# Performance work log

Measured on AMD Instinct MI355X. Metric: run time of the kernel, lower is better.

The kernel has to match this reference:

```python
import jax, jax.numpy as jnp
import numpy as np
from jax import lax

B, C, HW = 128, 32, 16
N_E = 4096
PNS = (1, 2, 3, 4, 5, 6, 8, 10, 13, 16)
SN = len(PNS)
BETA, RESI = 0.25, 0.5
EPS = 1e-12

# PhiPartiallyShared tick schedule (K=4): which of the 4 Phi convs each scale uses
_TICKS = np.linspace(1.0 / 12.0, 1.0 - 1.0 / 12.0, 4)
PHI_IDX = [int(np.argmin(np.abs(_TICKS - si / (SN - 1)))) for si in range(SN)]


def _cubic_w(t, a=-0.75):
    # PyTorch bicubic kernel (a = -0.75)
    t = np.abs(t)
    return np.where(t <= 1.0, ((a + 2.0) * t - (a + 3.0)) * t * t + 1.0,
                    np.where(t < 2.0, (((t - 5.0) * t + 8.0) * t - 4.0) * a, 0.0))


def _bicubic_mat(n_in, n_out):
    # 1D resize matrix matching F.interpolate(mode='bicubic', align_corners=False)
    M = np.zeros((n_out, n_in), np.float32)
    scale = n_in / n_out
    for i in range(n_out):
        src = (i + 0.5) * scale - 0.5
        i0 = int(np.floor(src))
        f = src - i0
        for off in (-1, 0, 1, 2):
            w = float(_cubic_w(f - off))
            j = min(max(i0 + off, 0), n_in - 1)  # border replicate
            M[i, j] += w
    return M


def _area_mat(n_in, n_out):
    # 1D matrix matching F.interpolate(mode='area') == adaptive_avg_pool
    M = np.zeros((n_out, n_in), np.float32)
    for i in range(n_out):
        s = (i * n_in) // n_out
        e = -(-((i + 1) * n_in) // n_out)  # ceil
        M[i, s:e] = 1.0 / (e - s)
    return M


DOWN = {pn: jnp.asarray(_area_mat(HW, pn)) for pn in PNS[:-1]}
UP = {pn: jnp.asarray(_bicubic_mat(pn, HW)) for pn in PNS[:-1]}


def _resize2(x, M):
    # separable 2D resize: x [B,C,Y,X] -> [B,C,O,P]
    return jnp.einsum('oy,px,bcyx->bcop', M, M, x)


def _phi(h, w, b):
    conv = lax.conv_general_dilated(h, w, (1, 1), ((1, 1), (1, 1)),
                                    dimension_numbers=('NCHW', 'OIHW', 'NCHW'))
    conv = conv + b[None, :, None, None]
    return h * (1.0 - RESI) + conv * RESI


def _forward(f_input, codebook, phi_w, phi_b):
    f_ng = lax.stop_gradient(f_input)
    f_rest = f_ng
    f_hat = jnp.zeros_like(f_ng)
    cb_n = codebook / jnp.maximum(jnp.linalg.norm(codebook, axis=-1, keepdims=True), EPS)
    loss = jnp.asarray(0.0, jnp.float32)
    idx = None
    for si, pn in enumerate(PNS):
        x = _resize2(f_rest, DOWN[pn]) if si != SN - 1 else f_rest
        rest = x.transpose(0, 2, 3, 1).reshape(-1, C)          # [B*pn*pn, C]
        rest_n = rest / jnp.maximum(jnp.linalg.norm(rest, axis=-1, keepdims=True), EPS)
        idx = jnp.argmax(rest_n @ cb_n.T, axis=1)              # cosine-sim argmax
        h = codebook[idx].reshape(B, pn, pn, C).transpose(0, 3, 1, 2)
        if si != SN - 1:
            h = _resize2(h, UP[pn])
        k = PHI_IDX[si]
        h = _phi(h, phi_w[k], phi_b[k])
        f_hat = f_hat + h
        f_rest = f_rest - h
        loss = loss + BETA * jnp.mean((lax.stop_gradient(f_hat) - f_input) ** 2) \
                    + jnp.mean((f_hat - f_ng) ** 2)
    loss = loss / SN
    # straight-through estimator
    f_hat_st = f_input + lax.stop_gradient(f_hat - f_input)
    return f_hat_st, loss, idx


def setup_inputs() -> dict:
    key = jax.random.key(0)
    k1, k2, k3, k4 = jax.random.split(key, 4)
    return {
        'f_input': jax.random.normal(k1, (B, C, HW, HW), jnp.float32),
        'codebook': jax.random.normal(k2, (N_E, C), jnp.float32) * 0.5,
        'phi_w': jax.random.normal(k3, (4, C, C, 3, 3), jnp.float32) * (1.0 / np.sqrt(C * 9)),
        'phi_b': jax.random.normal(k4, (4, C), jnp.float32) * 0.01,
    }


def reference(f_input, codebook, phi_w, phi_b):
    f_hat, loss, idx = _forward(f_input, codebook, phi_w, phi_b)
    # perplexity of last-scale code usage
    n_tok = idx.shape[0]
    avg_probs = jnp.zeros((N_E,), jnp.float32).at[idx].add(1.0) / n_tok
    perplexity = jnp.exp(-jnp.sum(avg_probs * jnp.log(avg_probs + 1e-10)))
    return f_hat, loss, perplexity
```

## Files before the change

### kernel.cpp

```cpp
#include <hip/hip_runtime.h>
#include <stdint.h>
#include <math.h>


#define DEVI __device__ __forceinline__

static constexpr int NE = 4096;

typedef _Float16 half8 __attribute__((ext_vector_type(8)));
typedef float floatx4 __attribute__((ext_vector_type(4)));

DEVI int imax(int a, int b) { return a > b ? a : b; }

DEVI float dppL(float v) {
    return __int_as_float(
        __builtin_amdgcn_update_dpp(0, __float_as_int(v), 0x111, 0xF, 0xF, true));
}
DEVI float dppR(float v) {
    return __int_as_float(
        __builtin_amdgcn_update_dpp(0, __float_as_int(v), 0x101, 0xF, 0xF, true));
}

__global__ void __launch_bounds__(256) k_setup(const float* __restrict__ cb,
                                               const float* __restrict__ pw,
                                               _Float16* __restrict__ cbh,
                                               _Float16* __restrict__ cbl,
                                               float* __restrict__ wT,
                                               float* __restrict__ um,
                                               float* __restrict__ lossAcc) {
    int blk = blockIdx.x, tid = threadIdx.x;
    if (blk < 16) {
        int r = blk * 256 + tid;
        const float* src = cb + r * 32;
        float v[32];
        float ss = 0.f;
#pragma unroll
        for (int j = 0; j < 32; ++j) { v[j] = src[j]; ss += v[j] * v[j]; }
        float n = fmaxf(sqrtf(ss), 1e-12f);
#pragma unroll
        for (int j = 0; j < 32; ++j) {
            float x = v[j] / n;
            _Float16 h = (_Float16)x;
            cbh[r * 32 + j] = h;
            cbl[r * 32 + j] = (_Float16)(x - (float)h);
        }
    } else if (blk < 160) {
        int e = (blk - 16) * 256 + tid;
        int k = e / 9216, rem = e % 9216;
        int q8 = rem / 1152, rem2 = rem % 1152;
        int ic = rem2 / 36, r3 = rem2 % 36;
        int k9 = r3 / 4, o2 = r3 % 4;
        int oc = (q8 >> 2) * 16 + (q8 & 3) * 4 + o2;
        int ky = k9 / 3, kx = k9 % 3;
        wT[e] = pw[(((k * 32 + oc) * 32 + ic) * 3 + ky) * 3 + kx];
    } else {
        if (tid < 144) {
            const int pns[9] = {1, 2, 3, 4, 5, 6, 8, 10, 13};
            int si = tid / 16, y = tid % 16, pn = pns[si];
            double scale = (double)pn / 16.0;
            double src = ((double)y + 0.5) * scale - 0.5;
            double fl = floor(src);
            int i0 = (int)fl;
            double f = src - fl;
            float row[13];
            for (int j = 0; j < pn; ++j) row[j] = 0.f;
            const double a = -0.75;
#pragma unroll
            for (int off = -1; off <= 2; ++off) {
                double t2 = fabs(f - (double)off);
                double wgt;
                if (t2 <= 1.0)      wgt = ((a + 2.0) * t2 - (a + 3.0)) * t2 * t2 + 1.0;
                else if (t2 < 2.0)  wgt = (((t2 - 5.0) * t2 + 8.0) * t2 - 4.0) * a;
                else                wgt = 0.0;
                int j = i0 + off;
                j = j < 0 ? 0 : (j > pn - 1 ? pn - 1 : j);
                row[j] = (float)((double)row[j] + wgt);
            }
            for (int j = 0; j < pn; ++j) um[si * 256 + y * pn + j] = row[j];
        } else {
            for (int i = tid - 144; i < 4112; i += 112) ((int*)lossAcc)[i] = 0;
        }
    }
}


template <int PN>
__global__ void __launch_bounds__(256) k_down(const float* __restrict__ src,
                                              _Float16* __restrict__ xh,
                                              _Float16* __restrict__ xl,
                                              unsigned long long* __restrict__ bestp) {
    constexpr int NT = PN * PN;
    constexpr int T = 128 * NT;
    constexpr int Tp = ((T + 511) / 512) * 512;
    int tid = threadIdx.x;
    for (int i = blockIdx.x * 256 + tid; i < Tp; i += gridDim.x * 256)
        bestp[i] = 0ull;
    if (blockIdx.x >= 256) {
        for (int i = tid; i < (Tp - T) * 32; i += 256) {
            xh[T * 32 + i] = (_Float16)0.f;
            xl[T * 32 + i] = (_Float16)0.f;
        }
        return;
    }
    __shared__ float r[16][260];
    int img = blockIdx.x >> 1, ch = (blockIdx.x & 1) * 16;

    const float4* s4 = (const float4*)(src + img * 8192 + ch * 256);
    for (int i = tid; i < 1024; i += 256) {
        float4 a = s4[i];
        int c = i >> 6, p = (i & 63) * 4;
        r[c][p]     = a.x;
        r[c][p + 1] = a.y;
        r[c][p + 2] = a.z;
        r[c][p + 3] = a.w;
    }
    __syncthreads();

    for (int e = tid; e < NT * 16; e += 256) {
        int lt = e >> 4, cp = e & 15;
        int oy = lt / PN, ox = lt % PN;
        int sy = oy * 16 / PN, ey = ((oy + 1) * 16 + PN - 1) / PN;
        int sx = ox * 16 / PN, ex = ((ox + 1) * 16 + PN - 1) / PN;
        float wy = 1.f / (float)(ey - sy);
        float wx = 1.f / (float)(ex - sx);
        float s = 0.f;
        for (int y = sy; y < ey; ++y)
            for (int x = sx; x < ex; ++x)
                s += r[cp][y * 16 + x];
        float v = s * (wy * wx);
        _Float16 h = (_Float16)v;
        int gid = (img * NT + lt) * 32 + ch + cp;
        xh[gid] = h;
        xl[gid] = (_Float16)(v - (float)h);
    }
}

template <int PN, int SEG>
__global__ void __launch_bounds__(256, 2) k_quant(
        const half8* __restrict__ xh, const half8* __restrict__ xl,
        const half8* __restrict__ cbh8, const half8* __restrict__ cbl8,
        unsigned long long* __restrict__ bestp) {
    constexpr int T = 128 * PN * PN;
    constexpr int Tp = ((T + 511) / 512) * 512;
    constexpr int TB = Tp / 512;
    constexpr int CPS = 4096 / SEG;
    static_assert(CPS == 128, "reg-streamed sweep sized for CPS==128");

    int tid = threadIdx.x;
    int bt = blockIdx.x % TB, seg = blockIdx.x / TB;
    int wv = tid >> 6, lane = tid & 63;
    int n0 = lane & 15, g = lane >> 4;
    int tokbase = bt * 512 + wv * 128;
    int cbase = seg * CPS;

    half8 ah[8], al[8];
#pragma unroll
    for (int mt = 0; mt < 8; ++mt) {
        int tok = tokbase + mt * 16 + n0;
        ah[mt] = xh[tok * 4 + g];
        al[mt] = xl[tok * 4 + g];
    }

    int mx[8];
#pragma unroll
    for (int mt = 0; mt < 8; ++mt) mx[mt] = (int)0x80000000;

    const floatx4 z4 = {0.f, 0.f, 0.f, 0.f};
    const int KMASK = ~(CPS - 1);
    int lowg = CPS - 1 - g * 4;

    int code0 = cbase + n0;
    half8 bh = cbh8[code0 * 4 + g];
    half8 bl = cbl8[code0 * 4 + g];
#pragma unroll 1
    for (int nt = 0; nt < 8; ++nt) {
        int nn = (nt + 1) & 7;
        int codeN = cbase + nn * 16 + n0;
        half8 bhn = cbh8[codeN * 4 + g];
        half8 bln = cbl8[codeN * 4 + g];
        int lowb = lowg - nt * 16;
#pragma unroll
        for (int mt = 0; mt < 8; ++mt) {
            floatx4 c;
            c = __builtin_amdgcn_mfma_f32_16x16x32_f16(bh, ah[mt], z4, 0, 0, 0);
            c = __builtin_amdgcn_mfma_f32_16x16x32_f16(bl, ah[mt], c,  0, 0, 0);
            c = __builtin_amdgcn_mfma_f32_16x16x32_f16(bh, al[mt], c,  0, 0, 0);
            int k0 = (__float_as_int(c[0]) & KMASK) | (lowb - 0);
            int k1 = (__float_as_int(c[1]) & KMASK) | (lowb - 1);
            int k2 = (__float_as_int(c[2]) & KMASK) | (lowb - 2);
            int k3 = (__float_as_int(c[3]) & KMASK) | (lowb - 3);
            mx[mt] = imax(mx[mt], imax(k0, k1));
            mx[mt] = imax(mx[mt], imax(k2, k3));
        }
        bh = bhn;
        bl = bln;
    }

#pragma unroll
    for (int mt = 0; mt < 8; ++mt) {
        int k = mx[mt];
        k = imax(k, __shfl_xor(k, 16, 64));
        k = imax(k, __shfl_xor(k, 32, 64));
        if (g == (mt >> 1)) {
            int gidx = cbase + (CPS - 1) - (k & (CPS - 1));
            unsigned long long k64 =
                ((unsigned long long)((unsigned)k ^ 0x80000000u) << 32) |
                (unsigned)~gidx;
            atomicMax(bestp + tokbase + mt * 16 + n0, k64);
        }
    }
}

template <int PN, int K, bool FIRST, bool LAST>
__global__ void __launch_bounds__(512) k_upconv(
        const float* __restrict__ fin, float* __restrict__ fhat,
        float* __restrict__ resid,
        const float* __restrict__ cbook,
        const unsigned long long* __restrict__ bestp,
        const float* __restrict__ wT, const float* __restrict__ phib,
        const float* __restrict__ um, float* __restrict__ lossAcc,
        int* __restrict__ hist, float* __restrict__ dout) {
    constexpr int NT = PN * PN;
    constexpr int RA = (PN < 16 && NT * 32 > 4096) ? NT * 32 : 4096;
    __shared__ __align__(16) float regionA[RA];
    __shared__ float hu1[(PN < 16) ? 32 * 6 * PN : 1];
    __shared__ float Us[(PN < 16) ? 16 * PN : 1];
    __shared__ int idxs[NT];
    __shared__ float red[8];
    float* S_hu = regionA;
    float* h0 = regionA;

    int img = blockIdx.x >> 2, q = blockIdx.x & 3;
    int y0 = q * 4;
    int tid = threadIdx.x;

    for (int e = tid; e < NT; e += 512) {
        unsigned long long k64 = bestp[img * NT + e];
        idxs[e] = (int)(~(unsigned)(k64 & 0xFFFFFFFFull));
    }
    if (PN < 16)
        for (int e = tid; e < 16 * PN; e += 512) Us[e] = um[e];
    __syncthreads();

    if (PN == 16) {
        if (LAST && tid < 64)
            atomicAdd(hist + idxs[y0 * 16 + tid], 1);
        for (int e = tid; e < 3072; e += 512) {
            int c = e / 96, r = e % 96;
            int rr = r >> 4, x = r & 15;
            int gy = y0 - 1 + rr;
            float v = 0.f;
            if (gy >= 0 && gy <= 15) v = cbook[idxs[gy * 16 + x] * 32 + c];
            S_hu[c * 128 + (rr + 1) * 16 + x] = v;
        }
    } else {
        for (int e = tid; e < NT * 32; e += 512) {
            int tk = e >> 5, c = e & 31;
            h0[e] = cbook[idxs[tk] * 32 + c];
        }
        __syncthreads();
        for (int e = tid; e < 6 * PN * 32; e += 512) {
            int c = e & 31, rest = e >> 5;
            int rr = rest / PN, i = rest % PN;
            int gy = y0 - 1 + rr;
            float s = 0.f;
            if (gy >= 0 && gy <= 15)
                for (int j = 0; j < PN; ++j)
                    s += Us[gy * PN + j] * h0[(j * PN + i) * 32 + c];
            hu1[(c * 6 + rr) * PN + i] = s;
        }
        __syncthreads();
        for (int e = tid; e < 3072; e += 512) {
            int c = e / 96, r = e % 96;
            int rr = r >> 4, x = r & 15;
            int gy = y0 - 1 + rr;
            float s = 0.f;
            if (gy >= 0 && gy <= 15)
                for (int i = 0; i < PN; ++i)
                    s += Us[x * PN + i] * hu1[(c * 6 + rr) * PN + i];
            S_hu[c * 128 + (rr + 1) * 16 + x] = s;
        }
    }
    __syncthreads();

    int px = tid & 63;
    int wvq = __builtin_amdgcn_readfirstlane(tid >> 6);
    int yo = px >> 4, x = px & 15;
    int y = y0 + yo;
    int ry = yo + 2;
    float acc[4] = {0.f, 0.f, 0.f, 0.f};
    const float* wk = wT + K * 9216 + wvq * 1152;
#pragma unroll 4
    for (int ic = 0; ic < 32; ++ic) {
        int a = ic * 128 + ry * 16 + x;
        float cm = S_hu[a - 16], cc = S_hu[a], cp = S_hu[a + 16];
        float lm = dppL(cm), lc = dppL(cc), lp = dppL(cp);
        float rm = dppR(cm), rc = dppR(cc), rp = dppR(cp);
        const float* w = wk + ic * 36;
#pragma unroll
        for (int o = 0; o < 4; ++o) {
            float s = acc[o];
            s = fmaf(w[o],      lm, s);
            s = fmaf(w[4 + o],  cm, s);
            s = fmaf(w[8 + o],  rm, s);
            s = fmaf(w[12 + o], lc, s);
            s = fmaf(w[16 + o], cc, s);
            s = fmaf(w[20 + o], rc, s);
            s = fmaf(w[24 + o], lp, s);
            s = fmaf(w[28 + o], cp, s);
            s = fmaf(w[32 + o], rp, s);
            acc[o] = s;
        }
    }

    float ss = 0.f;
    {
        int oc0 = (wvq >> 2) * 16 + (wvq & 3) * 4;
        int gbase = img * 8192 + oc0 * 256 + y * 16 + x;
        const float* bias = phib + K * 32 + oc0;
#pragma unroll
        for (int oi = 0; oi < 4; ++oi) {
            float conv = acc[oi] + bias[oi];
            float hval = 0.5f * S_hu[(oc0 + oi) * 128 + ry * 16 + x] + 0.5f * conv;
            float fh = (FIRST ? 0.f : fhat[gbase + oi * 256]) + hval;
            fhat[gbase + oi * 256] = fh;
            if (LAST) dout[gbase + oi * 256] = fh;
            float rr = fin[gbase + oi * 256] - fh;
            if (!LAST) resid[gbase + oi * 256] = rr;
            ss = fmaf(rr, rr, ss);
        }
    }
    int lane = tid & 63;
#pragma unroll
    for (int m = 1; m < 64; m <<= 1) ss += __shfl_xor(ss, m, 64);
    if (lane == 0) red[tid >> 6] = ss;
    __syncthreads();
    if (tid == 0)
        atomicAdd(lossAcc, red[0] + red[1] + red[2] + red[3] +
                           red[4] + red[5] + red[6] + red[7]);
}

__global__ void __launch_bounds__(256) k_final(const float* __restrict__ lossAcc,
                                               const int* __restrict__ hist,
                                               float* __restrict__ out) {
    __shared__ float red[256];
    int tid = threadIdx.x;
    float s = 0.f;
    for (int i = tid; i < 4096; i += 256) {
        float p = (float)hist[i] * (1.f / 32768.f);
        s += p * logf(p + 1e-10f);
    }
    red[tid] = s;
    __syncthreads();
    for (int k = 128; k > 0; k >>= 1) {
        if (tid < k) red[tid] += red[tid + k];
        __syncthreads();
    }
    if (tid == 0) {
        out[1048577] = expf(-red[0]);
        float L = 0.f;
        for (int si = 0; si < 10; ++si) L += lossAcc[si];
        out[1048576] = L * 1.25f / 1048576.f * 0.1f;
    }
}


extern "C" void kernel_launch(void* const* d_in, const int* in_sizes, int n_in,
                              void* d_out, int out_size, void* d_ws, size_t ws_size,
                              hipStream_t stream) {
    const float* f_in  = (const float*)d_in[0];
    const float* cbook = (const float*)d_in[1];
    const float* phiw  = (const float*)d_in[2];
    const float* phib  = (const float*)d_in[3];
    float* out = (float*)d_out;
    char* base = (char*)d_ws;

    float* fhat    = (float*)(base);
    float* lossAcc = (float*)(base + 4194304);
    int*   hist    = (int*)  (base + 4194368);
    float* wT      = (float*)(base + 4210752);
    float* um      = (float*)(base + 4358208);
    _Float16* cbh  = (_Float16*)(base + 4367424);
    _Float16* cbl  = (_Float16*)(base + 4629568);
    _Float16* xh   = (_Float16*)(base + 4891712);
    _Float16* xl   = (_Float16*)(base + 6988864);
    unsigned long long* bestp = (unsigned long long*)(base + 9086016);
    float* resid   = (float*)(base + 13280320);

    k_setup<<<161, 256, 0, stream>>>(cbook, phiw, cbh, cbl, wT, um, lossAcc);

#define SCALE(SI, PN, K, FIRST, LAST)                                                  \
    {                                                                                  \
        constexpr int T = 128 * PN * PN;                                               \
        constexpr int Tp = ((T + 511) / 512) * 512;                                    \
        constexpr int TB = Tp / 512;                                                   \
        constexpr int PADB = (Tp > T) ? 1 : 0;                                         \
        k_down<PN><<<256 + PADB, 256, 0, stream>>>(                                    \
            FIRST ? f_in : (const float*)resid, xh, xl, bestp);                        \
        k_quant<PN, 32><<<TB * 32, 256, 0, stream>>>(                                  \
            (const half8*)xh, (const half8*)xl, (const half8*)cbh,                     \
            (const half8*)cbl, bestp);                                                 \
        k_upconv<PN, K, FIRST, LAST><<<512, 512, 0, stream>>>(                         \
            f_in, fhat, resid, cbook, bestp, wT, phib, um + SI * 256,                  \
            lossAcc + SI, hist, out);                                                  \
    }
    SCALE(0, 1, 0, true, false);
    SCALE(1, 2, 0, false, false);
    SCALE(2, 3, 0, false, false);
    SCALE(3, 4, 1, false, false);
    SCALE(4, 5, 1, false, false);
    SCALE(5, 6, 2, false, false);
    SCALE(6, 8, 2, false, false);
    SCALE(7, 10, 2, false, false);
    SCALE(8, 13, 3, false, false);
    SCALE(9, 16, 3, false, true);
#undef SCALE
    k_final<<<1, 256, 0, stream>>>(lossAcc, hist, out);
}
```

Baseline: 455.8 us.

## Fuse area downsampling into quantizer for large scales, epoch-tag argmax keys

For the four largest scales, the separate downsample kernel is dropped and each quant block computes the area-pooled token features directly from the residual in registers. Per-scale zeroing of the best-match buffer is removed by packing an epoch number into the top bits of the 64-bit atomicMax key, so one clear in setup covers all scales. This saves kernel launches and an intermediate write and read, but each of the 32 codebook-segment blocks now recomputes the pooling redundantly from global memory. The key also loses low bits of score precision.

```diff
diff --git a/kernel.cpp b/kernel.cpp
--- a/kernel.cpp
+++ b/kernel.cpp
@@ -27,7 +27,8 @@
                                                _Float16* __restrict__ cbl,
                                                float* __restrict__ wT,
                                                float* __restrict__ um,
-                                               float* __restrict__ lossAcc) {
+                                               float* __restrict__ lossAcc,
+                                               unsigned long long* __restrict__ bestp) {
     int blk = blockIdx.x, tid = threadIdx.x;
     if (blk < 16) {
         int r = blk * 256 + tid;
@@ -53,7 +54,7 @@
         int oc = (q8 >> 2) * 16 + (q8 & 3) * 4 + o2;
         int ky = k9 / 3, kx = k9 % 3;
         wT[e] = pw[(((k * 32 + oc) * 32 + ic) * 3 + ky) * 3 + kx];
-    } else {
+    } else if (blk == 160) {
         if (tid < 144) {
             const int pns[9] = {1, 2, 3, 4, 5, 6, 8, 10, 13};
             int si = tid / 16, y = tid % 16, pn = pns[si];
@@ -80,6 +81,9 @@
         } else {
             for (int i = tid - 144; i < 4112; i += 112) ((int*)lossAcc)[i] = 0;
         }
+    } else {
+        for (int i = (blk - 161) * 256 + tid; i < 32768; i += 32 * 256)
+            bestp[i] = 0ull;
     }
 }
 
@@ -87,14 +91,11 @@
 template <int PN>
 __global__ void __launch_bounds__(256) k_down(const float* __restrict__ src,
                                               _Float16* __restrict__ xh,
-                                              _Float16* __restrict__ xl,
-                                              unsigned long long* __restrict__ bestp) {
+                                              _Float16* __restrict__ xl) {
     constexpr int NT = PN * PN;
     constexpr int T = 128 * NT;
     constexpr int Tp = ((T + 511) / 512) * 512;
     int tid = threadIdx.x;
-    for (int i = blockIdx.x * 256 + tid; i < Tp; i += gridDim.x * 256)
-        bestp[i] = 0ull;
     if (blockIdx.x >= 256) {
         for (int i = tid; i < (Tp - T) * 32; i += 256) {
             xh[T * 32 + i] = (_Float16)0.f;
@@ -135,16 +136,17 @@
     }
 }
 
-template <int PN, int SEG>
+template <int PN, int EPOCH, bool FUSED>
 __global__ void __launch_bounds__(256, 2) k_quant(
+        const float* __restrict__ src,
         const half8* __restrict__ xh, const half8* __restrict__ xl,
         const half8* __restrict__ cbh8, const half8* __restrict__ cbl8,
         unsigned long long* __restrict__ bestp) {
-    constexpr int T = 128 * PN * PN;
+    constexpr int NT = PN * PN;
+    constexpr int T = 128 * NT;
     constexpr int Tp = ((T + 511) / 512) * 512;
     constexpr int TB = Tp / 512;
-    constexpr int CPS = 4096 / SEG;
-    static_assert(CPS == 128, "reg-streamed sweep sized for CPS==128");
+    constexpr int CPS = 128;
 
     int tid = threadIdx.x;
     int bt = blockIdx.x % TB, seg = blockIdx.x / TB;
@@ -154,11 +156,46 @@
     int cbase = seg * CPS;
 
     half8 ah[8], al[8];
-#pragma unroll
-    for (int mt = 0; mt < 8; ++mt) {
-        int tok = tokbase + mt * 16 + n0;
-        ah[mt] = xh[tok * 4 + g];
-        al[mt] = xl[tok * 4 + g];
+    if constexpr (FUSED) {
+#pragma unroll
+        for (int mt = 0; mt < 8; ++mt) {
+            int tok = tokbase + mt * 16 + n0;
+            bool pad = false;
+            if constexpr (Tp != T) pad = (tok >= T);
+            if (pad) {
+#pragma unroll
+                for (int j = 0; j < 8; ++j) {
+                    ah[mt][j] = (_Float16)0.f;
+                    al[mt][j] = (_Float16)0.f;
+                }
+            } else {
+                int b = tok / NT, r = tok - b * NT;
+                int oy = r / PN, ox = r - oy * PN;
+                int sy = oy * 16 / PN, ey = ((oy + 1) * 16 + PN - 1) / PN;
+                int sx = ox * 16 / PN, ex = ((ox + 1) * 16 + PN - 1) / PN;
+                float wy = 1.f / (float)(ey - sy);
+                float wx = 1.f / (float)(ex - sx);
+                const float* sp = src + b * 8192 + (g * 8) * 256;
+#pragma unroll
+                for (int j = 0; j < 8; ++j) {
+                    float s = 0.f;
+                    for (int y = sy; y < ey; ++y)
+                        for (int x = sx; x < ex; ++x)
+                            s += sp[j * 256 + y * 16 + x];
+                    float v = s * (wy * wx);
+                    _Float16 h = (_Float16)v;
+                    ah[mt][j] = h;
+                    al[mt][j] = (_Float16)(v - (float)h);
+                }
+            }
+        }
+    } else {
+#pragma unroll
+        for (int mt = 0; mt < 8; ++mt) {
+            int tok = tokbase + mt * 16 + n0;
+            ah[mt] = xh[tok * 4 + g];
+            al[mt] = xl[tok * 4 + g];
+        }
     }
 
     int mx[8];
@@ -204,8 +241,9 @@
         if (g == (mt >> 1)) {
             int gidx = cbase + (CPS - 1) - (k & (CPS - 1));
             unsigned long long k64 =
-                ((unsigned long long)((unsigned)k ^ 0x80000000u) << 32) |
-                (unsigned)~gidx;
+                ((unsigned long long)EPOCH << 60) |
+                ((unsigned long long)((unsigned)k ^ 0x80000000u) << 28) |
+                (unsigned)(4095 - gidx);
             atomicMax(bestp + tokbase + mt * 16 + n0, k64);
         }
     }
@@ -236,7 +274,7 @@
 
     for (int e = tid; e < NT; e += 512) {
         unsigned long long k64 = bestp[img * NT + e];
-        idxs[e] = (int)(~(unsigned)(k64 & 0xFFFFFFFFull));
+        idxs[e] = 4095 - (int)(k64 & 0xFFFull);
     }
     if (PN < 16)
         for (int e = tid; e < 16 * PN; e += 512) Us[e] = um[e];
@@ -387,33 +425,47 @@
     unsigned long long* bestp = (unsigned long long*)(base + 9086016);
     float* resid   = (float*)(base + 13280320);
 
-    k_setup<<<161, 256, 0, stream>>>(cbook, phiw, cbh, cbl, wT, um, lossAcc);
-
-#define SCALE(SI, PN, K, FIRST, LAST)                                                  \
+    k_setup<<<193, 256, 0, stream>>>(cbook, phiw, cbh, cbl, wT, um, lossAcc,
+                                     bestp);
+
+#define SCALE_S(SI, PN, K, FIRST, LAST)                                                \
     {                                                                                  \
         constexpr int T = 128 * PN * PN;                                               \
         constexpr int Tp = ((T + 511) / 512) * 512;                                    \
         constexpr int TB = Tp / 512;                                                   \
         constexpr int PADB = (Tp > T) ? 1 : 0;                                         \
         k_down<PN><<<256 + PADB, 256, 0, stream>>>(                                    \
-            FIRST ? f_in : (const float*)resid, xh, xl, bestp);                        \
-        k_quant<PN, 32><<<TB * 32, 256, 0, stream>>>(                                  \
-            (const half8*)xh, (const half8*)xl, (const half8*)cbh,                     \
-            (const half8*)cbl, bestp);                                                 \
+            FIRST ? f_in : (const float*)resid, xh, xl);                               \
+        k_quant<PN, SI + 1, false><<<TB * 32, 256, 0, stream>>>(                       \
+            (const float*)resid, (const half8*)xh, (const half8*)xl,                   \
+            (const half8*)cbh, (const half8*)cbl, bestp);                              \
         k_upconv<PN, K, FIRST, LAST><<<512, 512, 0, stream>>>(                         \
             f_in, fhat, resid, cbook, bestp, wT, phib, um + SI * 256,                  \
             lossAcc + SI, hist, out);                                                  \
     }
-    SCALE(0, 1, 0, true, false);
-    SCALE(1, 2, 0, false, false);
-    SCALE(2, 3, 0, false, false);
-    SCALE(3, 4, 1, false, false);
-    SCALE(4, 5, 1, false, false);
-    SCALE(5, 6, 2, false, false);
-    SCALE(6, 8, 2, false, false);
-    SCALE(7, 10, 2, false, false);
-    SCALE(8, 13, 3, false, false);
-    SCALE(9, 16, 3, false, true);
-#undef SCALE
+#define SCALE_F(SI, PN, K, LAST)                                                       \
+    {                                                                                  \
+        constexpr int T = 128 * PN * PN;                                               \
+        constexpr int Tp = ((T + 511) / 512) * 512;                                    \
+        constexpr int TB = Tp / 512;                                                   \
+        k_quant<PN, SI + 1, true><<<TB * 32, 256, 0, stream>>>(                        \
+            (const float*)resid, (const half8*)xh, (const half8*)xl,                   \
+            (const half8*)cbh, (const half8*)cbl, bestp);                              \
+        k_upconv<PN, K, false, LAST><<<512, 512, 0, stream>>>(                         \
+            f_in, fhat, resid, cbook, bestp, wT, phib, um + SI * 256,                  \
+            lossAcc + SI, hist, out);                                                  \
+    }
+    SCALE_S(0, 1, 0, true, false);
+    SCALE_S(1, 2, 0, false, false);
+    SCALE_S(2, 3, 0, false, false);
+    SCALE_S(3, 4, 1, false, false);
+    SCALE_S(4, 5, 1, false, false);
+    SCALE_S(5, 6, 2, false, false);
+    SCALE_F(6, 8, 2, false);
+    SCALE_F(7, 10, 2, false);
+    SCALE_F(8, 13, 3, false);
+    SCALE_F(9, 16, 3, true);
+#undef SCALE_S
+#undef SCALE_F
     k_final<<<1, 256, 0, stream>>>(lossAcc, hist, out);
 }
```

Result: slower. 839.6 us (+84.2%).
